# Kernel tuning notes

Measured on AMD Instinct MI355X. Metric: run time of the kernel, lower is better.

Reference implementation:

```python
import jax, jax.numpy as jnp
import numpy as np

N_AGENTS = 32
N_HEADS = 8
HEAD_DIM = 32          # atten_dim // n_heads
HID = 256              # rnn_hidden_dim
ATT = 256              # atten_dim
N_ACT = 32
NEG = -1e9             # finite stand-in for -inf; exp underflows to 0 in softmax


def setup_inputs() -> dict:
    key = jax.random.key(0)
    ks = jax.random.split(key, 20)
    B, N, E = 4096, 64, 128
    w = lambda k, shape: (jax.random.normal(k, shape, jnp.float32) * 0.05)
    return {
        "inputs": jax.random.normal(ks[0], (B, N, E), jnp.float32),
        "hidden_state": jax.random.normal(ks[1], (B, N_AGENTS, HID), jnp.float32) * 0.1,
        "fc1_w": w(ks[2], (HID, E)), "fc1_b": jnp.zeros((HID,), jnp.float32),
        "q_w": w(ks[3], (ATT, HID)), "q_b": jnp.zeros((ATT,), jnp.float32),
        "k_w": w(ks[4], (ATT, HID)), "k_b": jnp.zeros((ATT,), jnp.float32),
        "v_w": w(ks[5], (ATT, HID)), "v_b": jnp.zeros((ATT,), jnp.float32),
        "w_ih": w(ks[6], (3 * HID, ATT)), "w_hh": w(ks[7], (3 * HID, HID)),
        "b_ih": jnp.zeros((3 * HID,), jnp.float32), "b_hh": jnp.zeros((3 * HID,), jnp.float32),
        "out_w": w(ks[8], (N_ACT, HID)), "out_b": jnp.zeros((N_ACT,), jnp.float32),
        "obs_mask": jax.random.randint(ks[9], (B, N, N), 0, 2).astype(bool),
        "scenario_mask": jax.random.randint(ks[10], (B, N_AGENTS), 0, 2).astype(bool),
    }


def reference(inputs, hidden_state, fc1_w, fc1_b, q_w, q_b, k_w, k_b, v_w, v_b,
              w_ih, w_hh, b_ih, b_hh, out_w, out_b, obs_mask, scenario_mask):
    B, N, _ = inputs.shape
    A, nh, e = N_AGENTS, N_HEADS, HEAD_DIM
    # fc1 + ReLU: [B, N, HID]
    x = jax.nn.relu(inputs @ fc1_w.T + fc1_b)
    # multi-head projections; queries only for the first A entities (agents)
    q = (x[:, :A] @ q_w.T + q_b).reshape(B, A, nh, e).transpose(0, 2, 1, 3)   # [B,nh,A,e]
    k = (x @ k_w.T + k_b).reshape(B, N, nh, e).transpose(0, 2, 3, 1)          # [B,nh,e,N]
    v = jax.nn.relu(x @ v_w.T + v_b).reshape(B, N, nh, e).transpose(0, 2, 1, 3)  # [B,nh,N,e]
    score = jnp.einsum('bhae,bhen->bhan', q, k) / np.float32(np.sqrt(e))      # [B,nh,A,N]
    m = obs_mask[:, :A, :][:, None, :, :]                                      # [B,1,A,N]
    score = jnp.where(m, NEG, score)
    w = jax.nn.softmax(score, axis=-1)
    # original: fully-masked rows give NaN then are zeroed; here zero all masked slots
    w = jnp.where(m, 0.0, w)
    att = jnp.einsum('bhan,bhne->bhae', w, v)                                  # [B,nh,A,e]
    att = att.transpose(0, 2, 1, 3).reshape(B * A, nh * e)                     # [B*A, ATT]
    # GRUCell step (PyTorch gate ordering: r, z, n)
    h0 = hidden_state.reshape(B * A, HID)
    gi = att @ w_ih.T + b_ih
    gh = h0 @ w_hh.T + b_hh
    ir, iz, in_ = jnp.split(gi, 3, axis=-1)
    hr, hz, hn = jnp.split(gh, 3, axis=-1)
    r = jax.nn.sigmoid(ir + hr)
    z = jax.nn.sigmoid(iz + hz)
    n = jnp.tanh(in_ + r * hn)
    h = (1.0 - z) * n + z * h0
    h = h.reshape(B, A, HID)
    am = scenario_mask[:, :, None]                                             # [B,A,1]
    h = jnp.where(am, 0.0, h)
    q_out = h @ out_w.T + out_b
    q_out = jnp.where(am, 0.0, q_out)
    return q_out, h
```

## Files before the change

### kernel.cpp

```cpp
#include <hip/hip_runtime.h>


using bfrag = __attribute__((ext_vector_type(8))) short;
using ffrag = __attribute__((ext_vector_type(4))) float;

#define MFMA(a,b,c) __builtin_amdgcn_mfma_f32_16x16x32_bf16((a),(b),(c),0,0,0)
#define SWZ(row,col,S,xm) ((row)*(S) + ((((col)&~7) ^ (((row)&(xm))<<3)) | ((col)&7)))

#define OFF_A2   0L
#define OFF_FC1  67108864L
#define OFF_QW   67141632L
#define OFF_KW   67207168L
#define OFF_VW   67272704L
#define OFF_WIH  67338240L
#define OFF_WHH  67534848L
#define OFF_OW   67731456L
#define OFF_FLAG 67739648L
#define WS_NEED_BYTES 135479552L

__device__ inline unsigned short f2bf(float x){
  union { float f; unsigned u; } v; v.f = x;
  unsigned r = v.u + 0x7fffu + ((v.u >> 16) & 1u);
  return (unsigned short)(r >> 16);
}
__device__ inline float bf2f(short b){
  union { unsigned u; float f; } v; v.u = ((unsigned)(unsigned short)b) << 16;
  return v.f;
}
__device__ inline bool getmask(const void* p, long i, int byteflag){
  return byteflag ? (((const unsigned char*)p)[i] != 0)
                  : (((const int*)p)[i] != 0);
}
__device__ inline ffrag fzero(){ ffrag z; z[0]=0.f; z[1]=0.f; z[2]=0.f; z[3]=0.f; return z; }

__global__ void k0_prep(const float* __restrict__ fc1, const float* __restrict__ qw,
    const float* __restrict__ kw, const float* __restrict__ vw, const float* __restrict__ wih,
    const float* __restrict__ whh, const float* __restrict__ ow, const float* __restrict__ h0,
    const void* __restrict__ obsm, short* __restrict__ ws){
  long tid = (long)blockIdx.x*blockDim.x + threadIdx.x;
  long n = (long)gridDim.x*blockDim.x;
  if (tid == 0){
    const int* mi = (const int*)obsm;
    int f = 0;
    for (int i=0;i<256;i++){ if ((unsigned)mi[i] > 1u){ f = 1; break; } }
    ((int*)(ws + OFF_FLAG))[0] = f;
  }
  for (long i=tid; i<32768; i+=n) ws[OFF_FC1+i] = (short)f2bf(fc1[i]);
  for (long i=tid; i<65536; i+=n){
    ws[OFF_QW+i] = (short)f2bf(qw[i]);
    ws[OFF_KW+i] = (short)f2bf(kw[i]);
    ws[OFF_VW+i] = (short)f2bf(vw[i]);
  }
  for (long i=tid; i<196608; i+=n){
    ws[OFF_WIH+i] = (short)f2bf(wih[i]);
    ws[OFF_WHH+i] = (short)f2bf(whh[i]);
  }
  for (long i=tid; i<8192; i+=n) ws[OFF_OW+i] = (short)f2bf(ow[i]);
  const float2* h2 = (const float2*)h0;
  unsigned* a2u = (unsigned*)(ws + OFF_A2);
  for (long i=tid; i<16777216L; i+=n){
    long row = i >> 7; int j = (int)(i & 127);
    float2 v = h2[i];
    unsigned pk = (unsigned)f2bf(v.x) | ((unsigned)f2bf(v.y) << 16);
    a2u[row*256 + 128 + j] = pk;
  }
}

__global__ __launch_bounds__(512) void k1_fqkv(const float* __restrict__ inp,
    const short* __restrict__ fc1B, const float* __restrict__ fc1_b,
    const short* __restrict__ wq, const short* __restrict__ wk, const short* __restrict__ wv,
    const float* __restrict__ qb, const float* __restrict__ kb, const float* __restrict__ vb,
    short* __restrict__ qC, short* __restrict__ kC, short* __restrict__ vC, int chunkB){
  __shared__ __align__(16) short smem[65536];
  short* a_s  = smem;
  short* fw_s = smem + 16384;
  short* x_s  = smem;
  int t = threadIdx.x;
  long R0 = (long)blockIdx.x * 128;
  long grow0 = (long)chunkB*65536 + R0;
  int lane = t&63, w = t>>6, lr = lane&15, ko = lane>>4;
  for (int i=0;i<4;i++){
    int c = t + i*512; int row = c>>4; int cc = (c&15)*8;
    const float* src = inp + (grow0 + row)*128 + cc;
    float4 f0 = *(const float4*)src; float4 f1 = *(const float4*)(src+4);
    bfrag v8;
    v8[0]=(short)f2bf(f0.x); v8[1]=(short)f2bf(f0.y); v8[2]=(short)f2bf(f0.z); v8[3]=(short)f2bf(f0.w);
    v8[4]=(short)f2bf(f1.x); v8[5]=(short)f2bf(f1.y); v8[6]=(short)f2bf(f1.z); v8[7]=(short)f2bf(f1.w);
    *(bfrag*)(a_s + SWZ(row, cc, 128, 7)) = v8;
  }
  for (int i=0;i<8;i++){
    int c = t + i*512; int row = c>>4; int cc = (c&15)*8;
    *(bfrag*)(fw_s + SWZ(row, cc, 128, 7)) = *(const bfrag*)(fc1B + row*128 + cc);
  }
  __syncthreads();
  ffrag acc1[16];
  #pragma unroll
  for (int i=0;i<16;i++) acc1[i]=fzero();
  for (int ks=0; ks<4; ks++){
    int kc = ks*32 + ko*8;
    bfrag a = *(const bfrag*)(a_s + SWZ(w*16+lr, kc, 128, 7));
    #pragma unroll
    for (int nt=0; nt<16; nt++){
      bfrag bb = *(const bfrag*)(fw_s + SWZ(nt*16+lr, kc, 128, 7));
      acc1[nt] = MFMA(a, bb, acc1[nt]);
    }
  }
  __syncthreads();
  #pragma unroll
  for (int nt=0; nt<16; nt++){
    float bias = fc1_b[nt*16+lr];
    #pragma unroll
    for (int r=0;r<4;r++){
      int row = w*16 + ko*4 + r;
      float v = acc1[nt][r] + bias; v = v>0.f?v:0.f;
      x_s[SWZ(row, nt*16+lr, 256, 7)] = (short)f2bf(v);
    }
  }
  bfrag a_r[8];
  #pragma unroll
  for (int ks=0; ks<8; ks++)
    a_r[ks] = *(const bfrag*)(x_s + SWZ(w*16+lr, ks*32+ko*8, 256, 7));
  auto STAGE2 = [&](int s){
    int kind = s>>2; int rb = (s&3)*64;
    const short* wsrc = (kind==0?wq:(kind==1?wk:wv)) + (long)rb*256;
    short* dst = smem + 32768 + (s&1)*16384;
    #pragma unroll
    for (int i=0;i<4;i++){
      int c = t + i*512; int row = c>>5; int cc = (c&31)*8;
      *(bfrag*)(dst + SWZ(row, cc, 256, 7)) = *(const bfrag*)(wsrc + (long)row*256 + cc);
    }
  };
  STAGE2(0);
  __syncthreads();
  for (int s=0; s<12; s++){
    if (s < 11) STAGE2(s+1);
    const short* wcur = smem + 32768 + (s&1)*16384;
    ffrag acc2[4];
    #pragma unroll
    for (int i=0;i<4;i++) acc2[i]=fzero();
    #pragma unroll
    for (int ks=0; ks<8; ks++){
      int kc = ks*32 + ko*8;
      #pragma unroll
      for (int nt=0; nt<4; nt++){
        bfrag bb = *(const bfrag*)(wcur + SWZ(nt*16+lr, kc, 256, 7));
        acc2[nt] = MFMA(a_r[ks], bb, acc2[nt]);
      }
    }
    int kind = s>>2; int rb = (s&3)*64;
    const float* bsrc = (kind==0?qb:(kind==1?kb:vb));
    #pragma unroll
    for (int nt=0; nt<4; nt++){
      int colk = rb + nt*16 + lr;
      float bias = bsrc[colk];
      #pragma unroll
      for (int r=0;r<4;r++){
        int row = w*16 + ko*4 + r;
        long rl = R0 + row;
        float v = acc2[nt][r] + bias;
        if (kind==0){
          if ((row&32)==0){
            long qrow = ((rl>>6)<<5) + (row&31);
            qC[qrow*256 + colk] = (short)f2bf(v);
          }
        } else if (kind==1){
          kC[rl*256 + colk] = (short)f2bf(v);
        } else {
          v = v>0.f?v:0.f;
          vC[rl*256 + colk] = (short)f2bf(v);
        }
      }
    }
    __syncthreads();
  }
}

__global__ __launch_bounds__(512,4) void k2_attn(const short* __restrict__ qC,
    const short* __restrict__ kC, const short* __restrict__ vC,
    const void* __restrict__ obsm, short* __restrict__ A2,
    const int* __restrict__ flagp, int chunkB){
  __shared__ __align__(16) short vT_s[8][2048];
  __shared__ __align__(16) short p_s[8][2048];
  __shared__ unsigned char m_s[2048];
  int t = threadIdx.x, bl = blockIdx.x;
  long b = (long)chunkB*1024 + bl;
  int lane = t&63, w = t>>6, lr = lane&15, ko = lane>>4;
  int mflag = *flagp;
  if (mflag){
    uchar4 mv = *(const uchar4*)((const unsigned char*)obsm + b*4096 + t*4);
    m_s[t*4]=mv.x; m_s[t*4+1]=mv.y; m_s[t*4+2]=mv.z; m_s[t*4+3]=mv.w;
  } else {
    int4 mv = *(const int4*)((const int*)obsm + b*4096 + t*4);
    m_s[t*4]  =(unsigned char)(mv.x!=0); m_s[t*4+1]=(unsigned char)(mv.y!=0);
    m_s[t*4+2]=(unsigned char)(mv.z!=0); m_s[t*4+3]=(unsigned char)(mv.w!=0);
  }
  const int h = w;
  const short* qh = qC + ((long)bl*32)*256 + h*32 + ko*8;
  bfrag a_q[2];
  #pragma unroll
  for (int mt=0; mt<2; mt++) a_q[mt] = *(const bfrag*)(qh + (mt*16+lr)*256);
  const short* kh = kC + ((long)bl*64)*256 + h*32 + ko*8;
  bfrag b_k[4];
  #pragma unroll
  for (int nt=0; nt<4; nt++) b_k[nt] = *(const bfrag*)(kh + (nt*16+lr)*256);
  #pragma unroll
  for (int i=0;i<4;i++){
    int n = i*16 + (lane>>2); int e0 = (lane&3)*8;
    bfrag vv = *(const bfrag*)(vC + ((long)bl*64 + n)*256 + h*32 + e0);
    #pragma unroll
    for (int j=0;j<8;j++) vT_s[w][SWZ(e0+j, n, 64, 7)] = vv[j];
  }
  ffrag sc[2][4];
  #pragma unroll
  for (int mt=0; mt<2; mt++)
    #pragma unroll
    for (int nt=0; nt<4; nt++) sc[mt][nt] = MFMA(a_q[mt], b_k[nt], fzero());
  __syncthreads();
  const float scale = 0.17677669529663687f;
  float rsi[2][4];
  #pragma unroll
  for (int mt=0; mt<2; mt++){
    #pragma unroll
    for (int r=0; r<4; r++){
      int arow = mt*16 + ko*4 + r;
      float sv[4]; int mk[4];
      #pragma unroll
      for (int nt=0; nt<4; nt++){
        mk[nt] = m_s[arow*64 + nt*16 + lr];
        sv[nt] = sc[mt][nt][r] * scale;
      }
      float mx = -3.0e38f;
      #pragma unroll
      for (int nt=0; nt<4; nt++) if (!mk[nt]) mx = fmaxf(mx, sv[nt]);
      for (int d=1; d<16; d<<=1) mx = fmaxf(mx, __shfl_xor(mx, d));
      float sum = 0.f;
      #pragma unroll
      for (int nt=0; nt<4; nt++){
        float p = mk[nt] ? 0.f : __expf(sv[nt]-mx);
        sv[nt] = p; sum += p;
      }
      for (int d=1; d<16; d<<=1) sum += __shfl_xor(sum, d);
      rsi[mt][r] = sum > 0.f ? 1.f/sum : 0.f;
      #pragma unroll
      for (int nt=0; nt<4; nt++)
        p_s[w][SWZ(arow, nt*16+lr, 64, 7)] = (short)f2bf(sv[nt]);
    }
  }
  ffrag o[2][2];
  #pragma unroll
  for (int mt=0;mt<2;mt++)
    #pragma unroll
    for (int nt=0;nt<2;nt++) o[mt][nt]=fzero();
  #pragma unroll
  for (int kk=0; kk<2; kk++){
    int kc = kk*32 + ko*8;
    bfrag pa0 = *(const bfrag*)(p_s[w]  + SWZ(lr,    kc, 64, 7));
    bfrag pa1 = *(const bfrag*)(p_s[w]  + SWZ(16+lr, kc, 64, 7));
    bfrag bv0 = *(const bfrag*)(vT_s[w] + SWZ(lr,    kc, 64, 7));
    bfrag bv1 = *(const bfrag*)(vT_s[w] + SWZ(16+lr, kc, 64, 7));
    o[0][0]=MFMA(pa0,bv0,o[0][0]); o[0][1]=MFMA(pa0,bv1,o[0][1]);
    o[1][0]=MFMA(pa1,bv0,o[1][0]); o[1][1]=MFMA(pa1,bv1,o[1][1]);
  }
  #pragma unroll
  for (int mt=0; mt<2; mt++)
    #pragma unroll
    for (int nt=0; nt<2; nt++)
      #pragma unroll
      for (int r=0; r<4; r++){
        int a = mt*16 + ko*4 + r;
        A2[((long)b*32 + a)*512 + h*32 + nt*16 + lr] = (short)f2bf(o[mt][nt][r]*rsi[mt][r]);
      }
}

__global__ __launch_bounds__(512) void k3_gru(const short* __restrict__ A2,
    const short* __restrict__ wihB, const short* __restrict__ whhB,
    const float* __restrict__ b_ih, const float* __restrict__ b_hh,
    const void* __restrict__ scen, float* __restrict__ hout, const int* __restrict__ flagp){
  __shared__ __align__(16) short w_s[2][24576];
  int t = threadIdx.x, bid = blockIdx.x;
  long R0 = (long)bid * 128;
  int mflag = *flagp;
  int lane = t&63, w = t>>6, lr = lane&15, ko = lane>>4;
  long rowbase = R0 + (long)w*16;
  auto STAGE = [&](int jb, int part){
    const short* base = part ? whhB : wihB;
    short* dst = w_s[part];
    #pragma unroll
    for (int i=0;i<6;i++){
      int c = t + i*512; int slab = c>>10; int cm = c&1023; int row = cm>>5; int cc = (cm&31)*8;
      *(bfrag*)(dst + slab*8192 + SWZ(row, cc, 256, 7)) =
          *(const bfrag*)(base + ((long)(slab*256 + jb*32 + row))*256 + cc);
    }
  };
  STAGE(0,0);
  const short* Ab = A2 + (rowbase + lr)*512 + ko*8;
  bfrag A[16];
  #pragma unroll
  for (int ks=0; ks<16; ks++)
    A[ks] = *(const bfrag*)(Ab + ks*32);
  __syncthreads();
  for (int jb=0; jb<8; jb++){
    ffrag aR[2], aZ[2], aI[2], aN[2];
    #pragma unroll
    for (int nt=0;nt<2;nt++){ aR[nt]=fzero(); aZ[nt]=fzero(); aI[nt]=fzero(); aN[nt]=fzero(); }
    STAGE(jb,1);
    {
      const short* wc = w_s[0];
      #pragma unroll
      for (int ks=0; ks<8; ks++){
        int kc = ks*32 + ko*8;
        #pragma unroll
        for (int nt=0; nt<2; nt++){
          bfrag bR = *(const bfrag*)(wc + 0*8192 + SWZ(nt*16+lr, kc, 256, 7));
          aR[nt] = MFMA(A[ks], bR, aR[nt]);
          bfrag bZ = *(const bfrag*)(wc + 1*8192 + SWZ(nt*16+lr, kc, 256, 7));
          aZ[nt] = MFMA(A[ks], bZ, aZ[nt]);
          bfrag bX = *(const bfrag*)(wc + 2*8192 + SWZ(nt*16+lr, kc, 256, 7));
          aI[nt] = MFMA(A[ks], bX, aI[nt]);
        }
      }
    }
    __syncthreads();
    if (jb < 7) STAGE(jb+1,0);
    {
      const short* wc = w_s[1];
      #pragma unroll
      for (int ks=0; ks<8; ks++){
        int kc = ks*32 + ko*8;
        #pragma unroll
        for (int nt=0; nt<2; nt++){
          bfrag bR = *(const bfrag*)(wc + 0*8192 + SWZ(nt*16+lr, kc, 256, 7));
          aR[nt] = MFMA(A[8+ks], bR, aR[nt]);
          bfrag bZ = *(const bfrag*)(wc + 1*8192 + SWZ(nt*16+lr, kc, 256, 7));
          aZ[nt] = MFMA(A[8+ks], bZ, aZ[nt]);
          bfrag bX = *(const bfrag*)(wc + 2*8192 + SWZ(nt*16+lr, kc, 256, 7));
          aN[nt] = MFMA(A[8+ks], bX, aN[nt]);
        }
      }
    }
    #pragma unroll
    for (int nt=0; nt<2; nt++){
      int j = jb*32 + nt*16 + lr;
      float bir = b_ih[j],     bhr = b_hh[j];
      float biz = b_ih[256+j], bhz = b_hh[256+j];
      float bin = b_ih[512+j], bhn = b_hh[512+j];
      #pragma unroll
      for (int rr=0; rr<4; rr++){
        long row = rowbase + ko*4 + rr;
        float rg = 1.f/(1.f + __expf(-(aR[nt][rr] + bir + bhr)));
        float zg = 1.f/(1.f + __expf(-(aZ[nt][rr] + biz + bhz)));
        float ag = aI[nt][rr] + bin + rg*(aN[nt][rr] + bhn);
        float ng = 2.f/(1.f + __expf(-2.f*ag)) - 1.f;
        float h0v = bf2f(A2[row*512 + 256 + j]);
        float hv = (1.f - zg)*ng + zg*h0v;
        if (getmask(scen, row, mflag)) hv = 0.f;
        hout[row*256 + j] = hv;
      }
    }
    __syncthreads();
  }
}

__global__ __launch_bounds__(512) void k4_out(const float* __restrict__ hout,
    const short* __restrict__ ow, const float* __restrict__ out_b,
    const void* __restrict__ scen, float* __restrict__ qout, const int* __restrict__ flagp){
  __shared__ __align__(16) short ow_s[32*256];
  int t = threadIdx.x; long R0 = (long)blockIdx.x * 256;
  int mflag = *flagp;
  for (int i=0;i<2;i++){
    int c = t + i*512; int row = c >> 5; int cc = (c & 31)*8;
    *(bfrag*)(ow_s + SWZ(row, cc, 256, 7)) = *(const bfrag*)(ow + row*256 + cc);
  }
  __syncthreads();
  int lane = t&63, w = t>>6, lr = lane&15, ko = lane>>4;
  ffrag acc[2][2];
  #pragma unroll
  for (int a=0;a<2;a++) for (int bq=0;bq<2;bq++) acc[a][bq]=fzero();
  for (int ks=0; ks<8; ks++){
    int kc = ks*32 + ko*8;
    #pragma unroll
    for (int mi=0; mi<2; mi++){
      long row = R0 + (w*2+mi)*16 + lr;
      const float* hp = hout + row*256 + kc;
      float4 f0 = *(const float4*)hp; float4 f1 = *(const float4*)(hp+4);
      bfrag a;
      a[0]=(short)f2bf(f0.x); a[1]=(short)f2bf(f0.y); a[2]=(short)f2bf(f0.z); a[3]=(short)f2bf(f0.w);
      a[4]=(short)f2bf(f1.x); a[5]=(short)f2bf(f1.y); a[6]=(short)f2bf(f1.z); a[7]=(short)f2bf(f1.w);
      #pragma unroll
      for (int nt=0; nt<2; nt++){
        bfrag bb = *(const bfrag*)(ow_s + SWZ(nt*16+lr, kc, 256, 7));
        acc[mi][nt] = MFMA(a, bb, acc[mi][nt]);
      }
    }
  }
  #pragma unroll
  for (int mi=0;mi<2;mi++)
    #pragma unroll
    for (int nt=0;nt<2;nt++){
      int col = nt*16 + lr;
      float ob = out_b[col];
      #pragma unroll
      for (int r=0;r<4;r++){
        long row = R0 + (w*2+mi)*16 + ko*4 + r;
        float qv = acc[mi][nt][r] + ob;
        if (getmask(scen, row, mflag)) qv = 0.f;
        qout[row*32 + col] = qv;
      }
    }
}

extern "C" void kernel_launch(void* const* d_in, const int* in_sizes, int n_in,
                              void* d_out, int out_size, void* d_ws, size_t ws_size,
                              hipStream_t stream){
  const float* inputs = (const float*)d_in[0];
  const float* hidden = (const float*)d_in[1];
  const float* fc1_w  = (const float*)d_in[2];
  const float* fc1_b  = (const float*)d_in[3];
  const float* q_w    = (const float*)d_in[4];
  const float* q_b    = (const float*)d_in[5];
  const float* k_w    = (const float*)d_in[6];
  const float* k_b    = (const float*)d_in[7];
  const float* v_w    = (const float*)d_in[8];
  const float* v_b    = (const float*)d_in[9];
  const float* w_ih   = (const float*)d_in[10];
  const float* w_hh   = (const float*)d_in[11];
  const float* b_ih   = (const float*)d_in[12];
  const float* b_hh   = (const float*)d_in[13];
  const float* out_w  = (const float*)d_in[14];
  const float* out_b  = (const float*)d_in[15];
  const void* obsm    = d_in[16];
  const void* scen    = d_in[17];
  (void)in_sizes; (void)n_in; (void)out_size;
  if ((long)ws_size < WS_NEED_BYTES) return;
  short* ws = (short*)d_ws;
  const int* flagp = (const int*)(ws + OFF_FLAG);
  float* qout = (float*)d_out;
  float* hout = qout + 4194304;
  short* qCs = (short*)qout;
  short* kCs = (short*)hout;
  short* vCs = kCs + 16777216L;
  short* A2  = ws + OFF_A2;

  hipLaunchKernelGGL(k0_prep, dim3(2048), dim3(256), 0, stream,
      fc1_w, q_w, k_w, v_w, w_ih, w_hh, out_w, hidden, obsm, ws);
  for (int c=0; c<4; c++){
    hipLaunchKernelGGL(k1_fqkv, dim3(512), dim3(512), 0, stream,
        inputs, ws + OFF_FC1, fc1_b, ws + OFF_QW, ws + OFF_KW, ws + OFF_VW,
        q_b, k_b, v_b, qCs, kCs, vCs, c);
    hipLaunchKernelGGL(k2_attn, dim3(1024), dim3(512), 0, stream,
        qCs, kCs, vCs, obsm, A2, flagp, c);
  }
  hipLaunchKernelGGL(k3_gru, dim3(1024), dim3(512), 0, stream,
      A2, ws + OFF_WIH, ws + OFF_WHH, b_ih, b_hh, scen, hout, flagp);
  hipLaunchKernelGGL(k4_out, dim3(512), dim3(512), 0, stream,
      hout, ws + OFF_OW, out_b, scen, qout, flagp);
}
```

Before: 644.4 us.

## Write Q into A2, halve chunk count, split GRU K across wave halves

The fc1/QKV kernel now writes Q directly into the A2 workspace slot that the attention output later overwrites. This frees the separate Q buffer, so K and V can use the whole hout region and the batch is processed in 2 larger chunks instead of 4, with fewer launches. The GRU kernel is restructured: each wave group covers 32 rows, and the input and hidden K-halves are computed by separate wave halves. Each weight fragment is reused across two row tiles, and the partial sums are combined through LDS. The trade-off is that the previous double-buffered weight staging is dropped, and extra LDS traffic and barriers are added per column block.

```diff
diff --git a/kernel.cpp b/kernel.cpp
--- a/kernel.cpp
+++ b/kernel.cpp
@@ -70,14 +70,14 @@
     const short* __restrict__ fc1B, const float* __restrict__ fc1_b,
     const short* __restrict__ wq, const short* __restrict__ wk, const short* __restrict__ wv,
     const float* __restrict__ qb, const float* __restrict__ kb, const float* __restrict__ vb,
-    short* __restrict__ qC, short* __restrict__ kC, short* __restrict__ vC, int chunkB){
+    short* __restrict__ A2, short* __restrict__ kC, short* __restrict__ vC, int chunkB){
   __shared__ __align__(16) short smem[65536];
   short* a_s  = smem;
   short* fw_s = smem + 16384;
   short* x_s  = smem;
   int t = threadIdx.x;
   long R0 = (long)blockIdx.x * 128;
-  long grow0 = (long)chunkB*65536 + R0;
+  long grow0 = (long)chunkB*131072 + R0;
   int lane = t&63, w = t>>6, lr = lane&15, ko = lane>>4;
   for (int i=0;i<4;i++){
     int c = t + i*512; int row = c>>4; int cc = (c&15)*8;
@@ -160,8 +160,9 @@
         float v = acc2[nt][r] + bias;
         if (kind==0){
           if ((row&32)==0){
-            long qrow = ((rl>>6)<<5) + (row&31);
-            qC[qrow*256 + colk] = (short)f2bf(v);
+            long grow = grow0 + row;
+            long qrow = ((grow>>6)<<5) + (grow&31);
+            A2[qrow*512 + colk] = (short)f2bf(v);
           }
         } else if (kind==1){
           kC[rl*256 + colk] = (short)f2bf(v);
@@ -175,15 +176,14 @@
   }
 }
 
-__global__ __launch_bounds__(512,4) void k2_attn(const short* __restrict__ qC,
-    const short* __restrict__ kC, const short* __restrict__ vC,
-    const void* __restrict__ obsm, short* __restrict__ A2,
+__global__ __launch_bounds__(512,4) void k2_attn(const short* __restrict__ kC,
+    const short* __restrict__ vC, const void* __restrict__ obsm, short* __restrict__ A2,
     const int* __restrict__ flagp, int chunkB){
   __shared__ __align__(16) short vT_s[8][2048];
   __shared__ __align__(16) short p_s[8][2048];
   __shared__ unsigned char m_s[2048];
   int t = threadIdx.x, bl = blockIdx.x;
-  long b = (long)chunkB*1024 + bl;
+  long b = (long)chunkB*2048 + bl;
   int lane = t&63, w = t>>6, lr = lane&15, ko = lane>>4;
   int mflag = *flagp;
   if (mflag){
@@ -195,10 +195,10 @@
     m_s[t*4+2]=(unsigned char)(mv.z!=0); m_s[t*4+3]=(unsigned char)(mv.w!=0);
   }
   const int h = w;
-  const short* qh = qC + ((long)bl*32)*256 + h*32 + ko*8;
+  const short* qh = A2 + ((long)b*32)*512 + h*32 + ko*8;
   bfrag a_q[2];
   #pragma unroll
-  for (int mt=0; mt<2; mt++) a_q[mt] = *(const bfrag*)(qh + (mt*16+lr)*256);
+  for (int mt=0; mt<2; mt++) a_q[mt] = *(const bfrag*)(qh + (long)(mt*16+lr)*512);
   const short* kh = kC + ((long)bl*64)*256 + h*32 + ko*8;
   bfrag b_k[4];
   #pragma unroll
@@ -276,88 +276,94 @@
     const short* __restrict__ wihB, const short* __restrict__ whhB,
     const float* __restrict__ b_ih, const float* __restrict__ b_hh,
     const void* __restrict__ scen, float* __restrict__ hout, const int* __restrict__ flagp){
-  __shared__ __align__(16) short w_s[2][24576];
+  __shared__ __align__(16) short w_s[49152];
+  __shared__ float part_s[4][48][64];
   int t = threadIdx.x, bid = blockIdx.x;
   long R0 = (long)bid * 128;
   int mflag = *flagp;
   int lane = t&63, w = t>>6, lr = lane&15, ko = lane>>4;
-  long rowbase = R0 + (long)w*16;
-  auto STAGE = [&](int jb, int part){
-    const short* base = part ? whhB : wihB;
-    short* dst = w_s[part];
-    #pragma unroll
-    for (int i=0;i<6;i++){
+  int g = w & 3, half = w >> 2;
+  long rowbase = R0 + (long)g*32;
+  const short* Ab = A2 + (rowbase + lr)*512 + half*256 + ko*8;
+  bfrag A[2][8];
+  #pragma unroll
+  for (int mt=0; mt<2; mt++)
+    #pragma unroll
+    for (int ks=0; ks<8; ks++)
+      A[mt][ks] = *(const bfrag*)(Ab + (long)mt*16*512 + ks*32);
+  const short* wc = w_s + half*24576;
+  for (int jb=0; jb<8; jb++){
+    #pragma unroll
+    for (int i=0;i<12;i++){
       int c = t + i*512; int slab = c>>10; int cm = c&1023; int row = cm>>5; int cc = (cm&31)*8;
-      *(bfrag*)(dst + slab*8192 + SWZ(row, cc, 256, 7)) =
-          *(const bfrag*)(base + ((long)(slab*256 + jb*32 + row))*256 + cc);
-    }
-  };
-  STAGE(0,0);
-  const short* Ab = A2 + (rowbase + lr)*512 + ko*8;
-  bfrag A[16];
-  #pragma unroll
-  for (int ks=0; ks<16; ks++)
-    A[ks] = *(const bfrag*)(Ab + ks*32);
-  __syncthreads();
-  for (int jb=0; jb<8; jb++){
-    ffrag aR[2], aZ[2], aI[2], aN[2];
-    #pragma unroll
-    for (int nt=0;nt<2;nt++){ aR[nt]=fzero(); aZ[nt]=fzero(); aI[nt]=fzero(); aN[nt]=fzero(); }
-    STAGE(jb,1);
-    {
-      const short* wc = w_s[0];
-      #pragma unroll
-      for (int ks=0; ks<8; ks++){
-        int kc = ks*32 + ko*8;
+      const short* src = (slab<3)
+        ? wihB + ((long)(slab*256 + jb*32 + row))*256 + cc
+        : whhB + ((long)((slab-3)*256 + jb*32 + row))*256 + cc;
+      *(bfrag*)(w_s + slab*8192 + SWZ(row, cc, 256, 7)) = *(const bfrag*)src;
+    }
+    __syncthreads();
+    ffrag aR[2][2], aZ[2][2], aX[2][2];
+    #pragma unroll
+    for (int nt=0;nt<2;nt++)
+      #pragma unroll
+      for (int mt=0;mt<2;mt++){ aR[nt][mt]=fzero(); aZ[nt][mt]=fzero(); aX[nt][mt]=fzero(); }
+    #pragma unroll
+    for (int ks=0; ks<8; ks++){
+      int kc = ks*32 + ko*8;
+      #pragma unroll
+      for (int nt=0; nt<2; nt++){
+        bfrag bR = *(const bfrag*)(wc + 0*8192 + SWZ(nt*16+lr, kc, 256, 7));
+        aR[nt][0] = MFMA(A[0][ks], bR, aR[nt][0]);
+        aR[nt][1] = MFMA(A[1][ks], bR, aR[nt][1]);
+        bfrag bZ = *(const bfrag*)(wc + 1*8192 + SWZ(nt*16+lr, kc, 256, 7));
+        aZ[nt][0] = MFMA(A[0][ks], bZ, aZ[nt][0]);
+        aZ[nt][1] = MFMA(A[1][ks], bZ, aZ[nt][1]);
+        bfrag bX = *(const bfrag*)(wc + 2*8192 + SWZ(nt*16+lr, kc, 256, 7));
+        aX[nt][0] = MFMA(A[0][ks], bX, aX[nt][0]);
+        aX[nt][1] = MFMA(A[1][ks], bX, aX[nt][1]);
+      }
+    }
+    if (half == 0){
+      #pragma unroll
+      for (int nt=0; nt<2; nt++)
         #pragma unroll
-        for (int nt=0; nt<2; nt++){
-          bfrag bR = *(const bfrag*)(wc + 0*8192 + SWZ(nt*16+lr, kc, 256, 7));
-          aR[nt] = MFMA(A[ks], bR, aR[nt]);
-          bfrag bZ = *(const bfrag*)(wc + 1*8192 + SWZ(nt*16+lr, kc, 256, 7));
-          aZ[nt] = MFMA(A[ks], bZ, aZ[nt]);
-          bfrag bX = *(const bfrag*)(wc + 2*8192 + SWZ(nt*16+lr, kc, 256, 7));
-          aI[nt] = MFMA(A[ks], bX, aI[nt]);
+        for (int mt=0; mt<2; mt++)
+          #pragma unroll
+          for (int rr=0; rr<4; rr++){
+            part_s[g][((0*2+nt)*2+mt)*4+rr][lane] = aR[nt][mt][rr];
+            part_s[g][((2+nt)*2+mt)*4+rr][lane]   = aZ[nt][mt][rr];
+            part_s[g][((4+nt)*2+mt)*4+rr][lane]   = aX[nt][mt][rr];
+          }
+    }
+    __syncthreads();
+    if (half == 1){
+      #pragma unroll
+      for (int nt=0; nt<2; nt++){
+        int j = jb*32 + nt*16 + lr;
+        float bir = b_ih[j],     bhr = b_hh[j];
+        float biz = b_ih[256+j], bhz = b_hh[256+j];
+        float bin = b_ih[512+j], bhn = b_hh[512+j];
+        #pragma unroll
+        for (int mt=0; mt<2; mt++){
+          #pragma unroll
+          for (int rr=0; rr<4; rr++){
+            float ir = part_s[g][((0*2+nt)*2+mt)*4+rr][lane];
+            float iz = part_s[g][((2+nt)*2+mt)*4+rr][lane];
+            float in_ = part_s[g][((4+nt)*2+mt)*4+rr][lane];
+            float hr = aR[nt][mt][rr], hz = aZ[nt][mt][rr], hn = aX[nt][mt][rr];
+            long row = rowbase + mt*16 + ko*4 + rr;
+            float rg = 1.f/(1.f + __expf(-(ir + hr + bir + bhr)));
+            float zg = 1.f/(1.f + __expf(-(iz + hz + biz + bhz)));
+            float ag = in_ + bin + rg*(hn + bhn);
+            float ng = 2.f/(1.f + __expf(-2.f*ag)) - 1.f;
+            float h0v = bf2f(A2[row*512 + 256 + j]);
+            float hv = (1.f - zg)*ng + zg*h0v;
+            if (getmask(scen, row, mflag)) hv = 0.f;
+            hout[row*256 + j] = hv;
+          }
         }
       }
     }
-    __syncthreads();
-    if (jb < 7) STAGE(jb+1,0);
-    {
-      const short* wc = w_s[1];
-      #pragma unroll
-      for (int ks=0; ks<8; ks++){
-        int kc = ks*32 + ko*8;
-        #pragma unroll
-        for (int nt=0; nt<2; nt++){
-          bfrag bR = *(const bfrag*)(wc + 0*8192 + SWZ(nt*16+lr, kc, 256, 7));
-          aR[nt] = MFMA(A[8+ks], bR, aR[nt]);
-          bfrag bZ = *(const bfrag*)(wc + 1*8192 + SWZ(nt*16+lr, kc, 256, 7));
-          aZ[nt] = MFMA(A[8+ks], bZ, aZ[nt]);
-          bfrag bX = *(const bfrag*)(wc + 2*8192 + SWZ(nt*16+lr, kc, 256, 7));
-          aN[nt] = MFMA(A[8+ks], bX, aN[nt]);
-        }
-      }
-    }
-    #pragma unroll
-    for (int nt=0; nt<2; nt++){
-      int j = jb*32 + nt*16 + lr;
-      float bir = b_ih[j],     bhr = b_hh[j];
-      float biz = b_ih[256+j], bhz = b_hh[256+j];
-      float bin = b_ih[512+j], bhn = b_hh[512+j];
-      #pragma unroll
-      for (int rr=0; rr<4; rr++){
-        long row = rowbase + ko*4 + rr;
-        float rg = 1.f/(1.f + __expf(-(aR[nt][rr] + bir + bhr)));
-        float zg = 1.f/(1.f + __expf(-(aZ[nt][rr] + biz + bhz)));
-        float ag = aI[nt][rr] + bin + rg*(aN[nt][rr] + bhn);
-        float ng = 2.f/(1.f + __expf(-2.f*ag)) - 1.f;
-        float h0v = bf2f(A2[row*512 + 256 + j]);
-        float hv = (1.f - zg)*ng + zg*h0v;
-        if (getmask(scen, row, mflag)) hv = 0.f;
-        hout[row*256 + j] = hv;
-      }
-    }
-    __syncthreads();
   }
 }
 
@@ -436,19 +442,18 @@
   const int* flagp = (const int*)(ws + OFF_FLAG);
   float* qout = (float*)d_out;
   float* hout = qout + 4194304;
-  short* qCs = (short*)qout;
   short* kCs = (short*)hout;
-  short* vCs = kCs + 16777216L;
+  short* vCs = kCs + 33554432L;
   short* A2  = ws + OFF_A2;
 
   hipLaunchKernelGGL(k0_prep, dim3(2048), dim3(256), 0, stream,
       fc1_w, q_w, k_w, v_w, w_ih, w_hh, out_w, hidden, obsm, ws);
-  for (int c=0; c<4; c++){
-    hipLaunchKernelGGL(k1_fqkv, dim3(512), dim3(512), 0, stream,
+  for (int c=0; c<2; c++){
+    hipLaunchKernelGGL(k1_fqkv, dim3(1024), dim3(512), 0, stream,
         inputs, ws + OFF_FC1, fc1_b, ws + OFF_QW, ws + OFF_KW, ws + OFF_VW,
-        q_b, k_b, v_b, qCs, kCs, vCs, c);
-    hipLaunchKernelGGL(k2_attn, dim3(1024), dim3(512), 0, stream,
-        qCs, kCs, vCs, obsm, A2, flagp, c);
+        q_b, k_b, v_b, A2, kCs, vCs, c);
+    hipLaunchKernelGGL(k2_attn, dim3(2048), dim3(512), 0, stream,
+        kCs, vCs, obsm, A2, flagp, c);
   }
   hipLaunchKernelGGL(k3_gru, dim3(1024), dim3(512), 0, stream,
       A2, ws + OFF_WIH, ws + OFF_WHH, b_ih, b_hh, scen, hout, flagp);
```

Result: slower. 694.5 us (+7.8%).

## Pre-swizzle GRU weights for direct LDS loads, store Q in A2, halve chunks

Applied to the files above, without the earlier changes.

The prep kernel now writes the GRU weights already tiled per jb block with the LDS XOR swizzle baked in. This lets k3 stage them with global_load_lds 16-byte direct copies instead of register round-trips. Q projections are written straight into the attention output buffer A2, which frees the output scratch so K/V chunks can be twice as large. The loop now runs 2 chunks of doubled grids instead of 4. This trades fewer launches and less staging work for larger scratch use and an in-place read/overwrite of A2 rows inside k2.

```diff
diff --git a/kernel.cpp b/kernel.cpp
--- a/kernel.cpp
+++ b/kernel.cpp
@@ -32,6 +32,10 @@
                   : (((const int*)p)[i] != 0);
 }
 __device__ inline ffrag fzero(){ ffrag z; z[0]=0.f; z[1]=0.f; z[2]=0.f; z[3]=0.f; return z; }
+__device__ inline void gload16(const short* g, short* l){
+  __builtin_amdgcn_global_load_lds((const __attribute__((address_space(1))) void*)g,
+                                   (__attribute__((address_space(3))) void*)l, 16, 0, 0);
+}
 
 __global__ void k0_prep(const float* __restrict__ fc1, const float* __restrict__ qw,
     const float* __restrict__ kw, const float* __restrict__ vw, const float* __restrict__ wih,
@@ -52,8 +56,12 @@
     ws[OFF_VW+i] = (short)f2bf(vw[i]);
   }
   for (long i=tid; i<196608; i+=n){
-    ws[OFF_WIH+i] = (short)f2bf(wih[i]);
-    ws[OFF_WHH+i] = (short)f2bf(whh[i]);
+    int R = (int)(i >> 8), c = (int)(i & 255);
+    int gate = R >> 8, grow = R & 255;
+    int jb = grow >> 5, row = grow & 31;
+    long dst = (long)((jb*3 + gate)*32 + row)*256 + (c ^ ((row&7)<<3));
+    ws[OFF_WIH + dst] = (short)f2bf(wih[i]);
+    ws[OFF_WHH + dst] = (short)f2bf(whh[i]);
   }
   for (long i=tid; i<8192; i+=n) ws[OFF_OW+i] = (short)f2bf(ow[i]);
   const float2* h2 = (const float2*)h0;
@@ -70,14 +78,14 @@
     const short* __restrict__ fc1B, const float* __restrict__ fc1_b,
     const short* __restrict__ wq, const short* __restrict__ wk, const short* __restrict__ wv,
     const float* __restrict__ qb, const float* __restrict__ kb, const float* __restrict__ vb,
-    short* __restrict__ qC, short* __restrict__ kC, short* __restrict__ vC, int chunkB){
+    short* __restrict__ A2, short* __restrict__ kC, short* __restrict__ vC, int chunkB){
   __shared__ __align__(16) short smem[65536];
   short* a_s  = smem;
   short* fw_s = smem + 16384;
   short* x_s  = smem;
   int t = threadIdx.x;
   long R0 = (long)blockIdx.x * 128;
-  long grow0 = (long)chunkB*65536 + R0;
+  long grow0 = (long)chunkB*131072 + R0;
   int lane = t&63, w = t>>6, lr = lane&15, ko = lane>>4;
   for (int i=0;i<4;i++){
     int c = t + i*512; int row = c>>4; int cc = (c&15)*8;
@@ -160,8 +168,9 @@
         float v = acc2[nt][r] + bias;
         if (kind==0){
           if ((row&32)==0){
-            long qrow = ((rl>>6)<<5) + (row&31);
-            qC[qrow*256 + colk] = (short)f2bf(v);
+            long grow = grow0 + row;
+            long qrow = ((grow>>6)<<5) + (grow&31);
+            A2[qrow*512 + colk] = (short)f2bf(v);
           }
         } else if (kind==1){
           kC[rl*256 + colk] = (short)f2bf(v);
@@ -175,15 +184,14 @@
   }
 }
 
-__global__ __launch_bounds__(512,4) void k2_attn(const short* __restrict__ qC,
-    const short* __restrict__ kC, const short* __restrict__ vC,
-    const void* __restrict__ obsm, short* __restrict__ A2,
+__global__ __launch_bounds__(512,4) void k2_attn(const short* __restrict__ kC,
+    const short* __restrict__ vC, const void* __restrict__ obsm, short* __restrict__ A2,
     const int* __restrict__ flagp, int chunkB){
   __shared__ __align__(16) short vT_s[8][2048];
   __shared__ __align__(16) short p_s[8][2048];
   __shared__ unsigned char m_s[2048];
   int t = threadIdx.x, bl = blockIdx.x;
-  long b = (long)chunkB*1024 + bl;
+  long b = (long)chunkB*2048 + bl;
   int lane = t&63, w = t>>6, lr = lane&15, ko = lane>>4;
   int mflag = *flagp;
   if (mflag){
@@ -195,10 +203,10 @@
     m_s[t*4+2]=(unsigned char)(mv.z!=0); m_s[t*4+3]=(unsigned char)(mv.w!=0);
   }
   const int h = w;
-  const short* qh = qC + ((long)bl*32)*256 + h*32 + ko*8;
+  const short* qh = A2 + ((long)b*32)*512 + h*32 + ko*8;
   bfrag a_q[2];
   #pragma unroll
-  for (int mt=0; mt<2; mt++) a_q[mt] = *(const bfrag*)(qh + (mt*16+lr)*256);
+  for (int mt=0; mt<2; mt++) a_q[mt] = *(const bfrag*)(qh + (long)(mt*16+lr)*512);
   const short* kh = kC + ((long)bl*64)*256 + h*32 + ko*8;
   bfrag b_k[4];
   #pragma unroll
@@ -273,7 +281,7 @@
 }
 
 __global__ __launch_bounds__(512) void k3_gru(const short* __restrict__ A2,
-    const short* __restrict__ wihB, const short* __restrict__ whhB,
+    const short* __restrict__ wihS, const short* __restrict__ whhS,
     const float* __restrict__ b_ih, const float* __restrict__ b_hh,
     const void* __restrict__ scen, float* __restrict__ hout, const int* __restrict__ flagp){
   __shared__ __align__(16) short w_s[2][24576];
@@ -283,14 +291,11 @@
   int lane = t&63, w = t>>6, lr = lane&15, ko = lane>>4;
   long rowbase = R0 + (long)w*16;
   auto STAGE = [&](int jb, int part){
-    const short* base = part ? whhB : wihB;
+    const short* src = (part ? whhS : wihS) + (long)jb*24576;
     short* dst = w_s[part];
     #pragma unroll
-    for (int i=0;i<6;i++){
-      int c = t + i*512; int slab = c>>10; int cm = c&1023; int row = cm>>5; int cc = (cm&31)*8;
-      *(bfrag*)(dst + slab*8192 + SWZ(row, cc, 256, 7)) =
-          *(const bfrag*)(base + ((long)(slab*256 + jb*32 + row))*256 + cc);
-    }
+    for (int i=0;i<6;i++)
+      gload16(src + (long)(i*512 + t)*8, dst + (i*512 + (t & ~63))*8);
   };
   STAGE(0,0);
   const short* Ab = A2 + (rowbase + lr)*512 + ko*8;
@@ -436,19 +441,18 @@
   const int* flagp = (const int*)(ws + OFF_FLAG);
   float* qout = (float*)d_out;
   float* hout = qout + 4194304;
-  short* qCs = (short*)qout;
   short* kCs = (short*)hout;
-  short* vCs = kCs + 16777216L;
+  short* vCs = kCs + 33554432L;
   short* A2  = ws + OFF_A2;
 
   hipLaunchKernelGGL(k0_prep, dim3(2048), dim3(256), 0, stream,
       fc1_w, q_w, k_w, v_w, w_ih, w_hh, out_w, hidden, obsm, ws);
-  for (int c=0; c<4; c++){
-    hipLaunchKernelGGL(k1_fqkv, dim3(512), dim3(512), 0, stream,
+  for (int c=0; c<2; c++){
+    hipLaunchKernelGGL(k1_fqkv, dim3(1024), dim3(512), 0, stream,
         inputs, ws + OFF_FC1, fc1_b, ws + OFF_QW, ws + OFF_KW, ws + OFF_VW,
-        q_b, k_b, v_b, qCs, kCs, vCs, c);
-    hipLaunchKernelGGL(k2_attn, dim3(1024), dim3(512), 0, stream,
-        qCs, kCs, vCs, obsm, A2, flagp, c);
+        q_b, k_b, v_b, A2, kCs, vCs, c);
+    hipLaunchKernelGGL(k2_attn, dim3(2048), dim3(512), 0, stream,
+        kCs, vCs, obsm, A2, flagp, c);
   }
   hipLaunchKernelGGL(k3_gru, dim3(1024), dim3(512), 0, stream,
       A2, ws + OFF_WIH, ws + OFF_WHH, b_ih, b_hh, scen, hout, flagp);
```

After: 612.8 us. 1.05x faster.
